# Kernel tuning notes

Measured on AMD Instinct MI355X. Metric: run time of the kernel, lower is better.

The kernel has to match this reference:

```python
import jax, jax.numpy as jnp
import numpy as np

#   x_out = Dy(alpha) @ J @ Dy(beta) @ J @ Dy(gamma) @ x   (per-irrep block diagonal)
# Dy(theta) is the sparse cos/sin y-rotation (exactly what encode_rotation_angle feeds
# into the segmented tensor product), and J = D(rotation by pi about (x+y)/sqrt(2)) is
# the constant Wigner matrix that conjugates a y-rotation into an x-rotation.

LMAX = 8
MUL = 64
LS = list(range(LMAX + 1))
DIM = MUL * sum(2 * l + 1 for l in LS)  # 5184
BATCH = 16384


def _so3_generators(l):
    # real antisymmetric so(3) generators for degree l (e3nn/cuE convention)
    m = np.arange(-l, l)
    raising = np.diag(-np.sqrt(l * (l + 1) - m * (m + 1)), k=-1).astype(np.complex128)
    m = np.arange(-l + 1, l + 1)
    lowering = np.diag(np.sqrt(l * (l + 1) - m * (m - 1)), k=1).astype(np.complex128)
    m = np.arange(-l, l + 1)
    X = np.stack([0.5 * (raising + lowering), np.diag(1j * m).astype(np.complex128),
                  -0.5j * (raising - lowering)])
    # change of basis complex -> real spherical harmonics
    q = np.zeros((2 * l + 1, 2 * l + 1), dtype=np.complex128)
    for mm in range(-l, 0):
        q[l + mm, l + abs(mm)] = 1.0 / np.sqrt(2)
        q[l + mm, l - abs(mm)] = -1j / np.sqrt(2)
    q[l, l] = 1.0
    for mm in range(1, l + 1):
        q[l + mm, l + abs(mm)] = (-1.0) ** mm / np.sqrt(2)
        q[l + mm, l - abs(mm)] = 1j * (-1.0) ** mm / np.sqrt(2)
    q = (-1j) ** l * q
    X = np.conj(q.T)[None] @ X @ q[None]
    return np.real(X)  # (3, 2l+1, 2l+1)


def _expm(A):
    w, V = np.linalg.eig(A.astype(np.complex128))
    return np.real(V @ np.diag(np.exp(w)) @ np.linalg.inv(V))


_J, _FREQ = [], []
for _l in LS:
    _X = _so3_generators(_l)
    # J = expm(pi * (Xx + Xy)/sqrt(2)): involution with J Dy(b) J = Dx(b)
    _J.append(jnp.asarray(_expm((np.pi / np.sqrt(2.0)) * (_X[0] + _X[1])), dtype=jnp.float32))
    _d = 2 * _l + 1
    # antidiagonal of the y-generator gives the per-row trig frequencies (+/- m)
    _FREQ.append(jnp.asarray(_X[1][np.arange(_d), _d - 1 - np.arange(_d)], dtype=jnp.float32))


def _rot_y(theta, freq, seg):
    # theta: [B], freq: [d], seg: [B, d, mul] (ir_mul layout)
    ang = freq * theta[:, None]                      # [B, d]
    return jnp.cos(ang)[..., None] * seg + jnp.sin(ang)[..., None] * seg[:, ::-1, :]


def setup_inputs() -> dict:
    key = jax.random.key(0)
    kg, kb, ka, kx = jax.random.split(key, 4)
    pi = float(np.pi)
    return {
        "gamma": jax.random.uniform(kg, (BATCH,), jnp.float32, -pi, pi),
        "beta": jax.random.uniform(kb, (BATCH,), jnp.float32, -pi, pi),
        "alpha": jax.random.uniform(ka, (BATCH,), jnp.float32, -pi, pi),
        "x": jax.random.normal(kx, (BATCH, DIM), jnp.float32),
    }


def reference(gamma, beta, alpha, x):
    outs = []
    off = 0
    for l, J, freq in zip(LS, _J, _FREQ):
        d = 2 * l + 1
        seg = x[:, off:off + d * MUL].reshape(-1, d, MUL)  # [B, 2l+1, mul]
        off += d * MUL
        seg = _rot_y(gamma, freq, seg)                      # first rotation about y
        seg = jnp.einsum('ij,bjm->bim', J, seg)
        seg = _rot_y(beta, freq, seg)                       # rotation about x (J-conjugated)
        seg = jnp.einsum('ij,bjm->bim', J, seg)
        seg = _rot_y(alpha, freq, seg)                      # last rotation about y
        outs.append(seg.reshape(-1, d * MUL))
    return jnp.concatenate(outs, axis=1)
```

## Files before the change

kernel.cpp:

```cpp
#include <hip/hip_runtime.h>
#include <math.h>
#include <complex>


#define LMAX 8
#define BATCH 16384
#define DIM 5184
#define NJ 969
#define NP 1140

__host__ __device__ constexpr int d_of(int l) { return 2 * l + 1; }
__host__ __device__ constexpr int joff_u(int l) {
    int o = 0;
    for (int k = 0; k < l; ++k) o += d_of(k) * d_of(k);
    return o;
}
__host__ __device__ constexpr int rp_of(int l) { return (d_of(l) + 3) & ~3; }
__host__ __device__ constexpr int poff_u(int l) {
    int o = 0;
    for (int k = 0; k < l; ++k) o += d_of(k) * rp_of(k);
    return o;
}

struct JPack { float v[NJ]; };

static void compute_J_host(JPack* jp) {
    for (int l = 0; l <= LMAX; ++l) {
        const int d = 2 * l + 1;
        std::complex<double> q[289], Ac[289], T1[289];
        double A[289], E[289], Tm[289], P[289];
        const double is2 = 1.0 / std::sqrt(2.0);
        static const double pr[4] = {1.0, 0.0, -1.0, 0.0};
        static const double pim[4] = {0.0, -1.0, 0.0, 1.0};
        const int ph = l & 3;
        for (int i = 0; i < d; ++i) {
            for (int j = 0; j < d; ++j) {
                double re = 0.0, im = 0.0;
                const int mm = i - l;
                if (mm < 0) {
                    if (j == l - mm) re = is2;
                    if (j == l + mm) im = -is2;
                } else if (mm == 0) {
                    if (j == l) re = 1.0;
                } else {
                    const double sgn = (mm & 1) ? -1.0 : 1.0;
                    if (j == l + mm) re = sgn * is2;
                    if (j == l - mm) im = sgn * is2;
                }
                q[i * d + j] = std::complex<double>(re * pr[ph] - im * pim[ph],
                                                    re * pim[ph] + im * pr[ph]);
                double xr = 0.0;
                if (j == i - 1) {
                    const double m = (double)(i - 1 - l);
                    xr += -0.5 * std::sqrt((double)l * (l + 1) - m * (m + 1));
                }
                if (j == i + 1) {
                    const double m = (double)(i - l + 1);
                    xr += 0.5 * std::sqrt((double)l * (l + 1) - m * (m - 1));
                }
                Ac[i * d + j] = std::complex<double>(xr, (i == j) ? (double)(i - l) : 0.0);
            }
        }
        for (int i = 0; i < d; ++i)
            for (int j = 0; j < d; ++j) {
                std::complex<double> s = 0.0;
                for (int k = 0; k < d; ++k) s += Ac[i * d + k] * q[k * d + j];
                T1[i * d + j] = s;
            }
        for (int i = 0; i < d; ++i)
            for (int j = 0; j < d; ++j) {
                std::complex<double> s = 0.0;
                for (int k = 0; k < d; ++k) s += std::conj(q[k * d + i]) * T1[k * d + j];
                A[i * d + j] = s.real() * (M_PI / std::sqrt(2.0));
            }
        double mx = 0.0;
        for (int i = 0; i < d; ++i) {
            double s = 0.0;
            for (int k = 0; k < d; ++k) s += std::fabs(A[i * d + k]);
            mx = std::fmax(mx, s);
        }
        int sh = 0;
        while (mx > 0.25 && sh < 60) { mx *= 0.5; ++sh; }
        const double sc = std::ldexp(1.0, -sh);
        for (int t = 0; t < d * d; ++t) A[t] *= sc;
        for (int i = 0; i < d; ++i)
            for (int j = 0; j < d; ++j) E[i * d + j] = Tm[i * d + j] = (i == j) ? 1.0 : 0.0;
        for (int kk = 1; kk <= 16; ++kk) {
            for (int i = 0; i < d; ++i)
                for (int j = 0; j < d; ++j) {
                    double s = 0.0;
                    for (int k = 0; k < d; ++k) s += Tm[i * d + k] * A[k * d + j];
                    P[i * d + j] = s / (double)kk;
                }
            for (int t = 0; t < d * d; ++t) { Tm[t] = P[t]; E[t] += P[t]; }
        }
        for (int q2 = 0; q2 < sh; ++q2) {
            for (int i = 0; i < d; ++i)
                for (int j = 0; j < d; ++j) {
                    double s = 0.0;
                    for (int k = 0; k < d; ++k) s += E[i * d + k] * E[k * d + j];
                    P[i * d + j] = s;
                }
            for (int t = 0; t < d * d; ++t) E[t] = P[t];
        }
        for (int i = 0; i < d; ++i)
            for (int j = 0; j < d; ++j)
                jp->v[joff_u(l) + i * d + j] = (float)E[i * d + j];
    }
}

__device__ __forceinline__ void wave_lds_fence() {
    asm volatile("s_waitcnt lgkmcnt(0)" ::: "memory");
    __builtin_amdgcn_sched_barrier(0);
}

template <int L>
__device__ __forceinline__ void stage_J(float* __restrict__ sJ, const float* __restrict__ Jg,
                                        int tid) {
    constexpr int d = d_of(L), RP = rp_of(L);
    const float* src = Jg + joff_u(L);
    float* dst = sJ + poff_u(L);
    for (int t = tid; t < d * d; t += 256) {
        const int i = t / d, j = t - i * d;
        dst[i * RP + j] = src[t];
    }
}

template <int L>
__device__ __forceinline__ void load_x(const float* __restrict__ xb, float* __restrict__ A) {
    constexpr int d = d_of(L);
    const float* p = xb + 64 * L * L;
#pragma unroll
    for (int i = 0; i < d; ++i) A[i] = p[i * 64];
}

template <int L, int PWOFF>
__device__ __forceinline__ void compose(const float* __restrict__ sJ,
                                        float* Dw,
                                        const float (&T)[3][2][17],
                                        int lane) {
    constexpr int d = d_of(L), h = (d + 1) / 2, RP = rp_of(L);
    const float* J = sJ + poff_u(L);
    float* D = Dw + poff_u(L);
    float* Pw = Dw + PWOFF;

    for (int t = lane; t < h * d; t += 64) {
        const int i = t / d, j = t - i * d;
        const int i2 = d - 1 - i, j2 = d - 1 - j;
        const float cg = T[0][0][(L - j) + 8], sg = T[0][1][(L - j) + 8];
        const float p1a = J[i * RP + j] * cg - J[i * RP + j2] * sg;
        const float p1b = J[i2 * RP + j] * cg - J[i2 * RP + j2] * sg;
        const float cb = T[1][0][(L - i) + 8], sb = T[1][1][(L - i) + 8];
        Pw[j * RP + i]  = cb * p1a + sb * p1b;
        Pw[j * RP + i2] = cb * p1b - sb * p1a;
    }
    wave_lds_fence();

    for (int t = lane; t < h * d; t += 64) {
        const int i = t / d, j = t - i * d;
        const int i2 = d - 1 - i;
        const float4* Ji  = reinterpret_cast<const float4*>(J + i * RP);
        const float4* Ji2 = reinterpret_cast<const float4*>(J + i2 * RP);
        const float4* Pj  = reinterpret_cast<const float4*>(Pw + j * RP);
        float ta = 0.f, tb = 0.f;
#pragma unroll
        for (int q = 0; q < RP / 4; ++q) {
            const float4 pv = Pj[q], ja = Ji[q], jb = Ji2[q];
            if (4 * q + 0 < d) { ta += ja.x * pv.x; tb += jb.x * pv.x; }
            if (4 * q + 1 < d) { ta += ja.y * pv.y; tb += jb.y * pv.y; }
            if (4 * q + 2 < d) { ta += ja.z * pv.z; tb += jb.z * pv.z; }
            if (4 * q + 3 < d) { ta += ja.w * pv.w; tb += jb.w * pv.w; }
        }
        const float ca = T[2][0][(L - i) + 8], sa = T[2][1][(L - i) + 8];
        D[i * RP + j]  = ca * ta + sa * tb;
        D[i2 * RP + j] = ca * tb - sa * ta;
    }
    wave_lds_fence();
}

template <int L>
__device__ __forceinline__ void apply(float* __restrict__ ob,
                                      const float* Dw,
                                      const float* __restrict__ A) {
    constexpr int d = d_of(L), RP = rp_of(L);
    const float* D = Dw + poff_u(L);
    float* o = ob + 64 * L * L;
#pragma unroll
    for (int i = 0; i < d; ++i) {
        const float4* row = reinterpret_cast<const float4*>(D + i * RP);
        float acc = 0.f;
#pragma unroll
        for (int q = 0; q < RP / 4; ++q) {
            const float4 f = row[q];
            if (4 * q + 0 < d) acc += f.x * A[4 * q + 0];
            if (4 * q + 1 < d) acc += f.y * A[4 * q + 1];
            if (4 * q + 2 < d) acc += f.z * A[4 * q + 2];
            if (4 * q + 3 < d) acc += f.w * A[4 * q + 3];
        }
        __builtin_nontemporal_store(acc, o + i * 64);
    }
}

__global__ __launch_bounds__(256) void rot_main(const float* __restrict__ gamma,
                                                const float* __restrict__ beta,
                                                const float* __restrict__ alpha,
                                                const float* __restrict__ x,
                                                float* __restrict__ out,
                                                const float* __restrict__ Jg) {
    __shared__ __align__(16) float sJ[NP];
    __shared__ __align__(16) float sD[4][NP];
    __shared__ float sT[4][3][2][17];

    const int tid = threadIdx.x;
    const int wave = tid >> 6, lane = tid & 63;
    const int b = blockIdx.x * 4 + wave;

    stage_J<0>(sJ, Jg, tid);
    stage_J<1>(sJ, Jg, tid);
    stage_J<2>(sJ, Jg, tid);
    stage_J<3>(sJ, Jg, tid);
    stage_J<4>(sJ, Jg, tid);
    stage_J<5>(sJ, Jg, tid);
    stage_J<6>(sJ, Jg, tid);
    stage_J<7>(sJ, Jg, tid);
    stage_J<8>(sJ, Jg, tid);

    if (lane < 51) {
        const int a = lane / 17, mm = lane - a * 17;
        const float th = (a == 0) ? gamma[b] : ((a == 1) ? beta[b] : alpha[b]);
        float s, c;
        __sincosf((float)(mm - 8) * th, &s, &c);
        sT[wave][a][0][mm] = c;
        sT[wave][a][1][mm] = s;
    }
    __syncthreads();

    const float (&T)[3][2][17] = sT[wave];
    float* Dw = sD[wave];

    const float* xb = x + (size_t)b * DIM + lane;
    float* ob = out + (size_t)b * DIM + lane;

    float A8[17], A7[15], A6[13], A5[11], A4[9], A3[7], A2[5], A1[3], A0[1];

    load_x<8>(xb, A8);
    load_x<7>(xb, A7);
    compose<8, 0>(sJ, Dw, T, lane);
    apply<8>(ob, Dw, A8);

    load_x<6>(xb, A6);
    compose<7, 800>(sJ, Dw, T, lane);
    apply<7>(ob, Dw, A7);

    load_x<5>(xb, A5);
    compose<6, 800>(sJ, Dw, T, lane);
    apply<6>(ob, Dw, A6);

    load_x<4>(xb, A4);
    compose<5, 800>(sJ, Dw, T, lane);
    apply<5>(ob, Dw, A5);

    load_x<3>(xb, A3);
    compose<4, 800>(sJ, Dw, T, lane);
    apply<4>(ob, Dw, A4);

    load_x<2>(xb, A2);
    compose<3, 800>(sJ, Dw, T, lane);
    apply<3>(ob, Dw, A3);

    load_x<1>(xb, A1);
    compose<2, 800>(sJ, Dw, T, lane);
    apply<2>(ob, Dw, A2);

    load_x<0>(xb, A0);
    compose<1, 800>(sJ, Dw, T, lane);
    apply<1>(ob, Dw, A1);

    compose<0, 800>(sJ, Dw, T, lane);
    apply<0>(ob, Dw, A0);
}

extern "C" void kernel_launch(void* const* d_in, const int* in_sizes, int n_in,
                              void* d_out, int out_size, void* d_ws, size_t ws_size,
                              hipStream_t stream) {
    const float* gamma = (const float*)d_in[0];
    const float* beta  = (const float*)d_in[1];
    const float* alpha = (const float*)d_in[2];
    const float* x     = (const float*)d_in[3];
    float* out = (float*)d_out;

    static JPack jp;
    static bool init = false;
    if (!init) { compute_J_host(&jp); init = true; }

    hipMemcpyAsync(d_ws, jp.v, sizeof(JPack), hipMemcpyHostToDevice, stream);

    hipLaunchKernelGGL(rot_main, dim3(BATCH / 4), dim3(256), 0, stream,
                       gamma, beta, alpha, x, out, (const float*)d_ws);
}
```

Baseline: 142.6 us.

## Stage output rows in LDS and emit 16-byte nontemporal vector stores; reverse degree order

Each wave's per-row scalar results are written into a padded LDS scratch area in chunks of eight rows, then re-read as float4 vectors so every lane issues 16-byte nontemporal stores covering contiguous output. The degree processing order is also reversed to go from l=0 up to l=8, with staging offsets chosen to avoid overwriting live composed matrices. The aim is fewer, wider global store transactions, at the cost of extra LDS traffic, wave fences and scheduling barriers. Reversing the order may also change register pressure, since the larger input arrays are now loaded later.

```diff
diff --git a/kernel.cpp b/kernel.cpp
--- a/kernel.cpp
+++ b/kernel.cpp
@@ -8,6 +8,8 @@
 #define DIM 5184
 #define NJ 969
 #define NP 1140
+
+typedef float nfloat4 __attribute__((ext_vector_type(4)));
 
 __host__ __device__ constexpr int d_of(int l) { return 2 * l + 1; }
 __host__ __device__ constexpr int joff_u(int l) {
@@ -178,26 +180,44 @@
     wave_lds_fence();
 }
 
-template <int L>
-__device__ __forceinline__ void apply(float* __restrict__ ob,
-                                      const float* Dw,
-                                      const float* __restrict__ A) {
+template <int L, int OSTG>
+__device__ __forceinline__ void apply(nfloat4* __restrict__ ob4, float* Dw,
+                                      const float* __restrict__ A, int lane) {
     constexpr int d = d_of(L), RP = rp_of(L);
+    constexpr int NS = (d + 3) / 4;
+    constexpr int NC = (NS + 1) / 2;
     const float* D = Dw + poff_u(L);
-    float* o = ob + 64 * L * L;
-#pragma unroll
-    for (int i = 0; i < d; ++i) {
-        const float4* row = reinterpret_cast<const float4*>(D + i * RP);
-        float acc = 0.f;
-#pragma unroll
-        for (int q = 0; q < RP / 4; ++q) {
-            const float4 f = row[q];
-            if (4 * q + 0 < d) acc += f.x * A[4 * q + 0];
-            if (4 * q + 1 < d) acc += f.y * A[4 * q + 1];
-            if (4 * q + 2 < d) acc += f.z * A[4 * q + 2];
-            if (4 * q + 3 < d) acc += f.w * A[4 * q + 3];
-        }
-        __builtin_nontemporal_store(acc, o + i * 64);
+    float* sX = Dw + OSTG;
+    const int r = lane >> 4, cg = lane & 15;
+    nfloat4* ob = ob4 + 16 * L * L;
+#pragma unroll
+    for (int c = 0; c < NC; ++c) {
+        const int i0 = 8 * c;
+        const int i1 = (8 * c + 8 < d) ? 8 * c + 8 : d;
+#pragma unroll
+        for (int i = i0; i < i1; ++i) {
+            const float4* row = reinterpret_cast<const float4*>(D + i * RP);
+            float acc = 0.f;
+#pragma unroll
+            for (int q = 0; q < RP / 4; ++q) {
+                const float4 f = row[q];
+                if (4 * q + 0 < d) acc += f.x * A[4 * q + 0];
+                if (4 * q + 1 < d) acc += f.y * A[4 * q + 1];
+                if (4 * q + 2 < d) acc += f.z * A[4 * q + 2];
+                if (4 * q + 3 < d) acc += f.w * A[4 * q + 3];
+            }
+            sX[(i - i0) * 68 + lane] = acc;
+        }
+        wave_lds_fence();
+#pragma unroll
+        for (int sl = 0; sl < 2; ++sl) {
+            const int s = 2 * c + sl;
+            if (s < NS && 4 * s + r < d) {
+                const nfloat4 v = *reinterpret_cast<const nfloat4*>(sX + (4 * sl + r) * 68 + 4 * cg);
+                __builtin_nontemporal_store(v, ob + 64 * s + lane);
+            }
+        }
+        __builtin_amdgcn_sched_barrier(0);
     }
 }
 
@@ -239,45 +259,45 @@
     float* Dw = sD[wave];
 
     const float* xb = x + (size_t)b * DIM + lane;
-    float* ob = out + (size_t)b * DIM + lane;
-
-    float A8[17], A7[15], A6[13], A5[11], A4[9], A3[7], A2[5], A1[3], A0[1];
+    nfloat4* ob4 = reinterpret_cast<nfloat4*>(out) + (size_t)b * (DIM / 4);
+
+    float A0[1], A1[3], A2[5], A3[7], A4[9], A5[11], A6[13], A7[15], A8[17];
+
+    load_x<0>(xb, A0);
+    load_x<1>(xb, A1);
+    compose<0, 800>(sJ, Dw, T, lane);
+    apply<0, 4>(ob4, Dw, A0, lane);
+
+    load_x<2>(xb, A2);
+    compose<1, 800>(sJ, Dw, T, lane);
+    apply<1, 16>(ob4, Dw, A1, lane);
+
+    load_x<3>(xb, A3);
+    compose<2, 800>(sJ, Dw, T, lane);
+    apply<2, 56>(ob4, Dw, A2, lane);
+
+    load_x<4>(xb, A4);
+    compose<3, 800>(sJ, Dw, T, lane);
+    apply<3, 112>(ob4, Dw, A3, lane);
+
+    load_x<5>(xb, A5);
+    compose<4, 800>(sJ, Dw, T, lane);
+    apply<4, 220>(ob4, Dw, A4, lane);
+
+    load_x<6>(xb, A6);
+    compose<5, 800>(sJ, Dw, T, lane);
+    apply<5, 352>(ob4, Dw, A5, lane);
+
+    load_x<7>(xb, A7);
+    compose<6, 800>(sJ, Dw, T, lane);
+    apply<6, 560>(ob4, Dw, A6, lane);
 
     load_x<8>(xb, A8);
-    load_x<7>(xb, A7);
+    compose<7, 800>(sJ, Dw, T, lane);
+    apply<7, 0>(ob4, Dw, A7, lane);
+
     compose<8, 0>(sJ, Dw, T, lane);
-    apply<8>(ob, Dw, A8);
-
-    load_x<6>(xb, A6);
-    compose<7, 800>(sJ, Dw, T, lane);
-    apply<7>(ob, Dw, A7);
-
-    load_x<5>(xb, A5);
-    compose<6, 800>(sJ, Dw, T, lane);
-    apply<6>(ob, Dw, A6);
-
-    load_x<4>(xb, A4);
-    compose<5, 800>(sJ, Dw, T, lane);
-    apply<5>(ob, Dw, A5);
-
-    load_x<3>(xb, A3);
-    compose<4, 800>(sJ, Dw, T, lane);
-    apply<4>(ob, Dw, A4);
-
-    load_x<2>(xb, A2);
-    compose<3, 800>(sJ, Dw, T, lane);
-    apply<3>(ob, Dw, A3);
-
-    load_x<1>(xb, A1);
-    compose<2, 800>(sJ, Dw, T, lane);
-    apply<2>(ob, Dw, A2);
-
-    load_x<0>(xb, A0);
-    compose<1, 800>(sJ, Dw, T, lane);
-    apply<1>(ob, Dw, A1);
-
-    compose<0, 800>(sJ, Dw, T, lane);
-    apply<0>(ob, Dw, A0);
+    apply<8, 0>(ob4, Dw, A8, lane);
 }
 
 extern "C" void kernel_launch(void* const* d_in, const int* in_sizes, int n_in,
@@ -293,7 +313,7 @@
     static bool init = false;
     if (!init) { compute_J_host(&jp); init = true; }
 
-    hipMemcpyAsync(d_ws, jp.v, sizeof(JPack), hipMemcpyHostToDevice, stream);
+    (void)hipMemcpyAsync(d_ws, jp.v, sizeof(JPack), hipMemcpyHostToDevice, stream);
 
     hipLaunchKernelGGL(rot_main, dim3(BATCH / 4), dim3(256), 0, stream,
                        gamma, beta, alpha, x, out, (const float*)d_ws);
```

New measurement: 144.5 us. Within noise of the previous version (+1.3%).
